# Optimization experiments

Hardware: AMD Instinct MI355X
Metric: run time of the kernel (lower is better)

Reference implementation:

```python
import jax, jax.numpy as jnp
import numpy as np

B, NCAMS = 1, 6
C_FEAT = 64                     # fusion_feat_in_dim
H, W = 88, 160                  # per-camera feature map size at fusion level
VOX_SIZE = (100, 100, 20)       # (x_dim, y_dim, z_dim) voxel counts
VOX_STR = (-50.0, -50.0, -15.0)
VOX_UNIT = (1.0, 1.0, 1.5)
N_VOX = VOX_SIZE[0] * VOX_SIZE[1] * VOX_SIZE[2]
EPS = 1e-8
V_PRE = 64                      # voxel_pre_dim[0]


def make_voxel_pts(dtype):
    # [B, 4, N]; homogeneous (x, y, z, 1) points, layout [z, y, x] flattened
    xs = jnp.linspace(VOX_STR[0], VOX_STR[0] + VOX_UNIT[0] * (VOX_SIZE[0] - 1), VOX_SIZE[0], dtype=dtype)
    ys = jnp.linspace(VOX_STR[1], VOX_STR[1] + VOX_UNIT[1] * (VOX_SIZE[1] - 1), VOX_SIZE[1], dtype=dtype)
    zs = jnp.linspace(VOX_STR[2], VOX_STR[2] + VOX_UNIT[2] * (VOX_SIZE[2] - 1), VOX_SIZE[2], dtype=dtype)
    zdim, ydim, xdim = VOX_SIZE[2], VOX_SIZE[1], VOX_SIZE[0]
    gx = jnp.broadcast_to(xs[None, None, :], (zdim, ydim, xdim)).reshape(-1)
    gy = jnp.broadcast_to(ys[None, :, None], (zdim, ydim, xdim)).reshape(-1)
    gz = jnp.broadcast_to(zs[:, None, None], (zdim, ydim, xdim)).reshape(-1)
    pts = jnp.stack([gx, gy, gz, jnp.ones_like(gx)], axis=0)  # [4, N]
    return jnp.broadcast_to(pts[None], (B, 4, N_VOX))


def _gather(imgf, iy, ix, Wd):
    # imgf: [BN, C, H*W]; iy/ix: [BN, N] int32 -> [BN, C, N]
    lin = iy * Wd + ix
    return jnp.take_along_axis(imgf, lin[:, None, :], axis=2)


def bilinear_sample(img, gx, gy):
    # grid_sample(mode='bilinear', padding_mode='zeros', align_corners=True)
    BN, C, Hd, Wd = img.shape
    x = (gx + 1.0) * 0.5 * (Wd - 1)
    y = (gy + 1.0) * 0.5 * (Hd - 1)
    x0 = jnp.floor(x); y0 = jnp.floor(y)
    wx1 = x - x0; wx0 = 1.0 - wx1
    wy1 = y - y0; wy0 = 1.0 - wy1
    imgf = img.reshape(BN, C, Hd * Wd)
    out = jnp.zeros((BN, C, gx.shape[1]), dtype=img.dtype)
    for xi, wxi in ((x0, wx0), (x0 + 1.0, wx1)):
        for yi, wyi in ((y0, wy0), (y0 + 1.0, wy1)):
            valid = (xi >= 0) & (xi <= Wd - 1) & (yi >= 0) & (yi <= Hd - 1)
            ii = jnp.clip(xi, 0, Wd - 1).astype(jnp.int32)
            jj = jnp.clip(yi, 0, Hd - 1).astype(jnp.int32)
            w = (wxi * wyi * valid.astype(img.dtype))[:, None, :]
            out = out + _gather(imgf, jj, ii, Wd) * w
    return out


def nearest_sample(img, gx, gy):
    # grid_sample(mode='nearest', padding_mode='zeros', align_corners=True)
    BN, C, Hd, Wd = img.shape
    x = (gx + 1.0) * 0.5 * (Wd - 1)
    y = (gy + 1.0) * 0.5 * (Hd - 1)
    xi = jnp.round(x); yi = jnp.round(y)
    valid = (xi >= 0) & (xi <= Wd - 1) & (yi >= 0) & (yi <= Hd - 1)
    ii = jnp.clip(xi, 0, Wd - 1).astype(jnp.int32)
    jj = jnp.clip(yi, 0, Hd - 1).astype(jnp.int32)
    imgf = img.reshape(BN, C, Hd * Wd)
    return _gather(imgf, jj, ii, Wd) * valid[:, None, :].astype(img.dtype)


def setup_inputs() -> dict:
    key = jax.random.key(0)
    ks = jax.random.split(key, 8)
    return {
        'multi_img_feat': jax.random.normal(ks[0], (B, NCAMS, C_FEAT, H, W), jnp.float32),
        'mask': jax.random.uniform(ks[1], (B, NCAMS, 1, H, W), jnp.float32),
        'K': jax.random.normal(ks[2], (B, NCAMS, 4, 4), jnp.float32),
        'extrinsics': jax.random.normal(ks[3], (B, NCAMS, 4, 4), jnp.float32),
        'w_no': jax.random.normal(ks[4], (V_PRE, C_FEAT + 1), jnp.float32) * 0.05,
        'b_no': jax.random.normal(ks[5], (V_PRE,), jnp.float32) * 0.05,
        'w_o': jax.random.normal(ks[6], (V_PRE, 2 * (C_FEAT + 1)), jnp.float32) * 0.05,
        'b_o': jax.random.normal(ks[7], (V_PRE,), jnp.float32) * 0.05,
    }


def reference(multi_img_feat, mask, K, extrinsics, w_no, b_no, w_o, b_o):
    Bb, NC, C, Hd, Wd = multi_img_feat.shape
    dt = multi_img_feat.dtype
    vpts = make_voxel_pts(dt)                                          # [B,4,N]
    vpts_c = jnp.broadcast_to(vpts[:, None], (Bb, NC, 4, N_VOX)).reshape(Bb * NC, 4, N_VOX)
    feats = multi_img_feat.reshape(Bb * NC, C, Hd, Wd)
    masks = mask.reshape(Bb * NC, 1, Hd, Wd)                           # interp to (H,W) is identity (same size, align_corners)
    ext = extrinsics.reshape(Bb * NC, 4, 4)[:, :3, :]
    K3 = K.reshape(Bb * NC, 4, 4)[:, :3, :3]

    v_local = jnp.einsum('bij,bjn->bin', ext, vpts_c)                  # [BN,3,N]
    cam_pts = jnp.einsum('bij,bjn->bin', K3, v_local)
    pix = cam_pts[:, :2] / (cam_pts[:, 2:3] + EPS)
    pix = jnp.where(jnp.all(jnp.isfinite(pix)), pix, jnp.clip(pix, -Wd * 2.0, Wd * 2.0))
    gx = (pix[:, 0] / (Wd - 1) - 0.5) * 2.0                            # [BN,N] normalized coords
    gy = (pix[:, 1] / (Hd - 1) - 0.5) * 2.0

    feat_w = bilinear_sample(feats, gx, gy)                            # [BN,C,N]
    m_occ = nearest_sample(masks, gx, gy) > 0.5                        # [BN,1,N]
    m_depth = v_local[:, 2:3] > 0
    oob = (gx > 1) | (gx < -1) | (gy > 1) | (gy < -1)
    valid = (m_occ & m_depth & (~oob)[:, None, :]).astype(dt)          # [BN,1,N]

    feat_w = jnp.concatenate([feat_w, v_local[:, 2:3] / VOX_SIZE[0]], axis=1) * valid  # [BN,C+1,N]

    feat_w = feat_w.reshape(Bb, NC, C + 1, N_VOX)
    valid = valid.reshape(Bb, NC, 1, N_VOX)
    count = valid.sum(axis=1)                                          # [B,1,N]

    # non-overlap branch: voxels seen by exactly one camera
    no_mask = (count == 1).astype(dt)
    vox_no = feat_w.sum(axis=1) * no_mask
    vox_no = jax.nn.elu(jnp.einsum('oc,bcn->bon', w_no, vox_no) + b_no[None, :, None]) * no_mask

    # overlap branch: cams {0,3,4} vs {1,2,5}
    o_mask = (count == 2).astype(dt)
    feat1 = feat_w[:, 0] + feat_w[:, 3] + feat_w[:, 4]
    feat2 = feat_w[:, 1] + feat_w[:, 2] + feat_w[:, 5]
    vox_o = jnp.concatenate([feat1, feat2], axis=1)                    # [B,2*(C+1),N]
    vox_o = jax.nn.elu(jnp.einsum('oc,bcn->bon', w_o, vox_o) + b_o[None, :, None]) * o_mask

    return vox_no + vox_o                                              # [B, V_PRE, N]
```

## Files before the change

kernel.cpp:

```cpp
#include <hip/hip_runtime.h>
#include <cmath>

#define NC 6
#define CF 64
#define HH 88
#define WW 160
#define NPIX 14080
#define NVOX 200000
#define VPRE 64
#define NGRP 782
#define NTRB 1320

typedef unsigned int u32;

#define FEATT_BYTES  (6u * 64u * 14080u * 4u)
#define CNT1_OFF     (FEATT_BYTES)
#define CNT2_OFF     (CNT1_OFF + 4096u)
#define REC1_OFF     (CNT2_OFF + 4096u)
#define REC2_OFF     (REC1_OFF + (u32)NVOX * 16u)
#define WS_NEED      ((size_t)REC2_OFF + (size_t)NVOX * 32u)
#define OCNT_OFF     (FEATT_BYTES)
#define OREC1_OFF    (OCNT_OFF + 256u)
#define OREC2_OFF    (OREC1_OFF + (u32)NVOX * 16u)
#define WS_NEED_OLD  ((size_t)OREC2_OFF + (size_t)NVOX * 32u)

__device__ __forceinline__ float elu1(float x) { return x > 0.0f ? x : expm1f(x); }

__device__ __forceinline__ float gather_bilin(const float* __restrict__ fsrc, int useT,
                                              int lane, int cam, float x, float y) {
    float x0f = floorf(x), y0f = floorf(y);
    float wx1 = x - x0f, wx0 = 1.0f - wx1;
    float wy1 = y - y0f, wy0 = 1.0f - wy1;
    float x1f = x0f + 1.0f, y1f = y0f + 1.0f;
    float bx0 = (x0f >= 0.0f && x0f <= 159.0f) ? 1.0f : 0.0f;
    float bx1 = (x1f >= 0.0f && x1f <= 159.0f) ? 1.0f : 0.0f;
    float by0 = (y0f >= 0.0f && y0f <= 87.0f) ? 1.0f : 0.0f;
    float by1 = (y1f >= 0.0f && y1f <= 87.0f) ? 1.0f : 0.0f;
    int ix0 = (int)fminf(fmaxf(x0f, 0.0f), 159.0f);
    int ix1 = (int)fminf(fmaxf(x1f, 0.0f), 159.0f);
    int iy0 = (int)fminf(fmaxf(y0f, 0.0f), 87.0f);
    int iy1 = (int)fminf(fmaxf(y1f, 0.0f), 87.0f);
    int A = useT ? 64 : 1;
    int Boff = useT ? (cam * NPIX * 64 + lane) : ((cam * 64 + lane) * NPIX);
    float v00 = fsrc[(iy0 * WW + ix0) * A + Boff];
    float v01 = fsrc[(iy1 * WW + ix0) * A + Boff];
    float v10 = fsrc[(iy0 * WW + ix1) * A + Boff];
    float v11 = fsrc[(iy1 * WW + ix1) * A + Boff];
    float fv;
    fv  = (wx0 * wy0 * bx0 * by0) * v00;
    fv += (wx0 * wy1 * bx0 * by1) * v01;
    fv += (wx1 * wy0 * bx1 * by0) * v10;
    fv += (wx1 * wy1 * bx1 * by1) * v11;
    return fv;
}

__global__ __launch_bounds__(256) void vox_prep(
    const float* __restrict__ feats,
    float* __restrict__ featT,
    const float* __restrict__ mask,
    const float* __restrict__ Kg,
    const float* __restrict__ ext,
    float* __restrict__ outp,
    float4* __restrict__ rec1,
    float4* __restrict__ rec2,
    int* __restrict__ cnt1g,
    int* __restrict__ cnt2g)
{
    __shared__ __align__(16) float s_buf[4290];
    __shared__ float s_ext[72];
    __shared__ float s_K[54];
    __shared__ int s_c1, s_c2;

    int tid = threadIdx.x;
    int lane = tid & 63;
    int wv = tid >> 6;
    int bid = blockIdx.x;

    if (bid < NTRB) {
        int c = bid / 220;
        int p0 = (bid - c * 220) * 64;
        for (int r = wv; r < 64; r += 4)
            s_buf[r * 65 + lane] = feats[(c * 64 + r) * NPIX + p0 + lane];
        __syncthreads();
        for (int r = wv; r < 64; r += 4)
            featT[((c * NPIX) + p0 + r) * 64 + lane] = s_buf[lane * 65 + r];
    } else {
        int g = bid - NTRB;
        float4* s_r1 = (float4*)s_buf;
        float4* s_r2 = ((float4*)s_buf) + 256;
        if (tid == 0) { s_c1 = 0; s_c2 = 0; }
        if (tid >= 64 && tid < 136) {
            int i = tid - 64;
            s_ext[i] = ext[(i / 12) * 16 + (i % 12)];
        }
        if (tid >= 160 && tid < 214) {
            int i = tid - 160; int cam = i / 9; int e = i - cam * 9;
            s_K[i] = Kg[cam * 16 + (e / 3) * 4 + (e % 3)];
        }
        __syncthreads();
        int n = g * 256 + tid;
        if (n < NVOX) {
            #pragma clang fp contract(off)
            int xi = n % 100;
            int t = n / 100;
            int yi = t % 100;
            int zi = t / 100;
            float X = -50.0f + (float)xi;
            float Y = -50.0f + (float)yi;
            float Z = -15.0f + 1.5f * (float)zi;
            int cc = 0, cam0 = 0, cam1 = 0;
            float ax = 0.f, ay = 0.f, az = 0.f, bx = 0.f, by = 0.f, bz = 0.f;
            #pragma unroll
            for (int cam = 0; cam < NC; ++cam) {
                const float* E = s_ext + cam * 12;
                const float* Kk = s_K + cam * 9;
                float vl0 = E[0]*X + E[1]*Y + E[2]*Z + E[3];
                float vl1 = E[4]*X + E[5]*Y + E[6]*Z + E[7];
                float vl2 = E[8]*X + E[9]*Y + E[10]*Z + E[11];
                float c0 = Kk[0]*vl0 + Kk[1]*vl1 + Kk[2]*vl2;
                float c1 = Kk[3]*vl0 + Kk[4]*vl1 + Kk[5]*vl2;
                float c2 = Kk[6]*vl0 + Kk[7]*vl1 + Kk[8]*vl2;
                float pz = c2 + 1e-8f;
                float px = c0 / pz;
                float py = c1 / pz;
                float gx = (px / 159.0f - 0.5f) * 2.0f;
                float gy = (py / 87.0f - 0.5f) * 2.0f;
                float x = ((gx + 1.0f) * 0.5f) * 159.0f;
                float y = ((gy + 1.0f) * 0.5f) * 87.0f;
                float xr = rintf(x), yr = rintf(y);
                bool nv = (xr >= 0.0f) && (xr <= 159.0f) && (yr >= 0.0f) && (yr <= 87.0f);
                float mval = 0.0f;
                if (nv) mval = mask[(cam * HH + (int)yr) * WW + (int)xr];
                bool ok = (mval > 0.5f) && (vl2 > 0.0f) &&
                          !((gx > 1.0f) || (gx < -1.0f) || (gy > 1.0f) || (gy < -1.0f));
                if (ok) {
                    if (cc == 0) { ax = x; ay = y; az = vl2; cam0 = cam; }
                    else if (cc == 1) { bx = x; by = y; bz = vl2; cam1 = cam; }
                    ++cc;
                }
            }
            if (cc == 1) {
                int s = atomicAdd(&s_c1, 1);
                s_r1[s] = make_float4(ax, ay, az, __int_as_float((n << 3) | cam0));
            } else if (cc == 2) {
                int s = atomicAdd(&s_c2, 1);
                s_r2[2 * s + 0] = make_float4(ax, ay, az, __int_as_float((n << 3) | cam0));
                s_r2[2 * s + 1] = make_float4(bx, by, bz, __int_as_float((n << 3) | cam1));
            }
        }
        __syncthreads();
        int c1 = s_c1, c2 = s_c2;
        if (tid == 0) { cnt1g[g] = c1; cnt2g[g] = c2; }
        for (int i = tid; i < c1; i += 256) rec1[g * 256 + i] = s_r1[i];
        for (int i = tid; i < 2 * c2; i += 256) rec2[g * 512 + i] = s_r2[i];
    }

    {
        float4* o4 = (float4*)outp;
        const int n4 = VPRE * NVOX / 4;
        const int stride = (NTRB + NGRP) * 256;
        for (int i = bid * 256 + tid; i < n4; i += stride)
            o4[i] = make_float4(0.f, 0.f, 0.f, 0.f);
    }
}

__device__ __forceinline__ void scan_counts(const int* __restrict__ cg,
                                            int* s_scr, int* s_P, int tid) {
    int base = tid * 4;
    int v0 = (base + 0 < NGRP) ? cg[base + 0] : 0;
    int v1 = (base + 1 < NGRP) ? cg[base + 1] : 0;
    int v2 = (base + 2 < NGRP) ? cg[base + 2] : 0;
    int v3 = (base + 3 < NGRP) ? cg[base + 3] : 0;
    int s0 = v0, s1 = s0 + v1, s2 = s1 + v2, s3 = s2 + v3;
    s_scr[tid] = s3;
    __syncthreads();
    for (int off = 1; off < 256; off <<= 1) {
        int x = s_scr[tid];
        int y = (tid >= off) ? s_scr[tid - off] : 0;
        __syncthreads();
        s_scr[tid] = x + y;
        __syncthreads();
    }
    int excl = (tid > 0) ? s_scr[tid - 1] : 0;
    if (base + 0 < NGRP) s_P[base + 0] = excl + s0;
    if (base + 1 < NGRP) s_P[base + 1] = excl + s1;
    if (base + 2 < NGRP) s_P[base + 2] = excl + s2;
    if (base + 3 < NGRP) s_P[base + 3] = excl + s3;
    __syncthreads();
}

__device__ __forceinline__ int bsearch_grp(const int* __restrict__ P, int k) {
    int lo = 0, hi = NGRP - 1;
    while (lo < hi) { int mid = (lo + hi) >> 1; if (P[mid] > k) hi = mid; else lo = mid + 1; }
    return lo;
}

__global__ __launch_bounds__(256) void vox_comp2(
    const float* __restrict__ featT,
    const float* __restrict__ wno,
    const float* __restrict__ bno,
    const float* __restrict__ wo,
    const float* __restrict__ bo,
    float* __restrict__ outp,
    const float4* __restrict__ rec1,
    const float4* __restrict__ rec2,
    const int* __restrict__ cnt1g,
    const int* __restrict__ cnt2g)
{
    __shared__ float s_F[65 * 66];
    __shared__ float4 s_rec[128];
    __shared__ int s_vox[64];
    __shared__ int s_P1[NGRP];
    __shared__ int s_P2[NGRP];

    int tid = threadIdx.x;
    int lane = tid & 63;
    int wv = tid >> 6;
    int wvu = __builtin_amdgcn_readfirstlane(wv);
    int obase = wvu * 16;

    scan_counts(cnt1g, (int*)s_F, s_P1, tid);
    scan_counts(cnt2g, (int*)s_F, s_P2, tid);
    int n1 = s_P1[NGRP - 1], n2 = s_P2[NGRP - 1];
    int T1 = (n1 + 63) >> 6;
    int T2 = (n2 + 63) >> 6;
    int TT = T1 + T2;

    for (int t = blockIdx.x; t < TT; t += gridDim.x) {
        if (t < T1) {
            int e0 = t << 6;
            int tl = min(64, n1 - e0);
            if (tid < tl) {
                int k = e0 + tid;
                int g = bsearch_grp(s_P1, k);
                int l = k - ((g > 0) ? s_P1[g - 1] : 0);
                s_rec[tid] = rec1[g * 256 + l];
            }
            __syncthreads();
            for (int e = wv; e < tl; e += 4) {
                float4 r = s_rec[e];
                int meta = __float_as_int(r.w);
                int cam = meta & 7;
                float fv = gather_bilin(featT, 1, lane, cam, r.x, r.y);
                s_F[lane * 66 + e] = fv;
                if (lane == 0) { s_F[64 * 66 + e] = r.z / 100.0f; s_vox[e] = meta >> 3; }
            }
            __syncthreads();
            float acc[16];
            #pragma unroll
            for (int o = 0; o < 16; ++o) acc[o] = bno[obase + o];
            for (int cg2 = 0; cg2 < 64; cg2 += 4) {
                float f0 = s_F[(cg2 + 0) * 66 + lane];
                float f1 = s_F[(cg2 + 1) * 66 + lane];
                float f2 = s_F[(cg2 + 2) * 66 + lane];
                float f3 = s_F[(cg2 + 3) * 66 + lane];
                #pragma unroll
                for (int o = 0; o < 16; ++o) {
                    const float* wr = wno + (obase + o) * 65 + cg2;
                    acc[o] += wr[0] * f0; acc[o] += wr[1] * f1;
                    acc[o] += wr[2] * f2; acc[o] += wr[3] * f3;
                }
            }
            {
                float fd = s_F[64 * 66 + lane];
                #pragma unroll
                for (int o = 0; o < 16; ++o) acc[o] += wno[(obase + o) * 65 + 64] * fd;
            }
            if (lane < tl) {
                size_t col = (size_t)s_vox[lane];
                #pragma unroll
                for (int o = 0; o < 16; ++o)
                    outp[(size_t)(obase + o) * NVOX + col] = elu1(acc[o]);
            }
            __syncthreads();
        } else {
            int tt = t - T1;
            int e0 = tt << 6;
            int tl = min(64, n2 - e0);
            if (tid < 2 * tl) {
                int p = tid >> 1, h = tid & 1;
                int k = e0 + p;
                int g = bsearch_grp(s_P2, k);
                int l = k - ((g > 0) ? s_P2[g - 1] : 0);
                s_rec[tid] = rec2[g * 512 + 2 * l + h];
            }
            __syncthreads();
            for (int e = wv; e < tl; e += 4) {
                float4 r0 = s_rec[2 * e + 0];
                float4 r1 = s_rec[2 * e + 1];
                int m0 = __float_as_int(r0.w), m1 = __float_as_int(r1.w);
                int ca = m0 & 7, cb = m1 & 7;
                float fg = 0.0f, dd = 0.0f;
                if (!(ca == 1 || ca == 2 || ca == 5)) {
                    fg += gather_bilin(featT, 1, lane, ca, r0.x, r0.y);
                    dd += r0.z / 100.0f;
                }
                if (!(cb == 1 || cb == 2 || cb == 5)) {
                    fg += gather_bilin(featT, 1, lane, cb, r1.x, r1.y);
                    dd += r1.z / 100.0f;
                }
                s_F[lane * 66 + e] = fg;
                if (lane == 0) { s_F[64 * 66 + e] = dd; s_vox[e] = m0 >> 3; }
            }
            __syncthreads();
            float acc[16];
            #pragma unroll
            for (int o = 0; o < 16; ++o) acc[o] = bo[obase + o];
            for (int cg2 = 0; cg2 < 64; cg2 += 4) {
                float f0 = s_F[(cg2 + 0) * 66 + lane];
                float f1 = s_F[(cg2 + 1) * 66 + lane];
                float f2 = s_F[(cg2 + 2) * 66 + lane];
                float f3 = s_F[(cg2 + 3) * 66 + lane];
                #pragma unroll
                for (int o = 0; o < 16; ++o) {
                    const float* wr = wo + (obase + o) * 130 + cg2;
                    acc[o] += wr[0] * f0; acc[o] += wr[1] * f1;
                    acc[o] += wr[2] * f2; acc[o] += wr[3] * f3;
                }
            }
            {
                float fd = s_F[64 * 66 + lane];
                #pragma unroll
                for (int o = 0; o < 16; ++o) acc[o] += wo[(obase + o) * 130 + 64] * fd;
            }
            __syncthreads();
            for (int e = wv; e < tl; e += 4) {
                float4 r0 = s_rec[2 * e + 0];
                float4 r1 = s_rec[2 * e + 1];
                int m0 = __float_as_int(r0.w), m1 = __float_as_int(r1.w);
                int ca = m0 & 7, cb = m1 & 7;
                float fg = 0.0f, dd = 0.0f;
                if (ca == 1 || ca == 2 || ca == 5) {
                    fg += gather_bilin(featT, 1, lane, ca, r0.x, r0.y);
                    dd += r0.z / 100.0f;
                }
                if (cb == 1 || cb == 2 || cb == 5) {
                    fg += gather_bilin(featT, 1, lane, cb, r1.x, r1.y);
                    dd += r1.z / 100.0f;
                }
                s_F[lane * 66 + e] = fg;
                if (lane == 0) s_F[64 * 66 + e] = dd;
            }
            __syncthreads();
            for (int cg2 = 0; cg2 < 64; cg2 += 4) {
                float f0 = s_F[(cg2 + 0) * 66 + lane];
                float f1 = s_F[(cg2 + 1) * 66 + lane];
                float f2 = s_F[(cg2 + 2) * 66 + lane];
                float f3 = s_F[(cg2 + 3) * 66 + lane];
                #pragma unroll
                for (int o = 0; o < 16; ++o) {
                    const float* wr = wo + (obase + o) * 130 + 65 + cg2;
                    acc[o] += wr[0] * f0; acc[o] += wr[1] * f1;
                    acc[o] += wr[2] * f2; acc[o] += wr[3] * f3;
                }
            }
            {
                float fd = s_F[64 * 66 + lane];
                #pragma unroll
                for (int o = 0; o < 16; ++o) acc[o] += wo[(obase + o) * 130 + 129] * fd;
            }
            if (lane < tl) {
                size_t col = (size_t)s_vox[lane];
                #pragma unroll
                for (int o = 0; o < 16; ++o)
                    outp[(size_t)(obase + o) * NVOX + col] = elu1(acc[o]);
            }
            __syncthreads();
        }
    }
}

__global__ __launch_bounds__(256) void zero_out(float4* __restrict__ p, int n4) {
    int i = blockIdx.x * 256 + threadIdx.x;
    int stride = gridDim.x * 256;
    for (; i < n4; i += stride)
        p[i] = make_float4(0.f, 0.f, 0.f, 0.f);
}

__global__ __launch_bounds__(256) void transpose_feats(const float* __restrict__ in,
                                                       float* __restrict__ out,
                                                       int* __restrict__ cnt) {
    __shared__ float tile[64 * 65];
    if (cnt && blockIdx.x == 0 && threadIdx.x < 2) cnt[threadIdx.x] = 0;
    int blk = blockIdx.x;
    int c = blk / 220;
    int p0 = (blk - c * 220) * 64;
    int tid = threadIdx.x;
    int lane = tid & 63;
    int quad = tid >> 6;
    for (int r = quad; r < 64; r += 4)
        tile[r * 65 + lane] = in[(c * 64 + r) * NPIX + p0 + lane];
    __syncthreads();
    for (int r = quad; r < 64; r += 4)
        out[((c * NPIX) + p0 + r) * 64 + lane] = tile[lane * 65 + r];
}

__global__ __launch_bounds__(256) void vox_geom(
    const float* __restrict__ mask,
    const float* __restrict__ Kg,
    const float* __restrict__ ext,
    float4* __restrict__ rec1,
    float4* __restrict__ rec2,
    int* __restrict__ cnt)
{
    __shared__ float s_ext[72];
    __shared__ float s_K[54];
    __shared__ float4 s_r1[256];
    __shared__ float4 s_r2[512];
    __shared__ int s_c1, s_c2, s_b1, s_b2;

    int tid = threadIdx.x;
    if (tid == 0) { s_c1 = 0; s_c2 = 0; }
    if (tid >= 64 && tid < 136) {
        int i = tid - 64;
        s_ext[i] = ext[(i / 12) * 16 + (i % 12)];
    }
    if (tid >= 160 && tid < 214) {
        int i = tid - 160; int cam = i / 9; int e = i - cam * 9;
        s_K[i] = Kg[cam * 16 + (e / 3) * 4 + (e % 3)];
    }
    __syncthreads();

    int n = blockIdx.x * 256 + tid;
    if (n < NVOX) {
        #pragma clang fp contract(off)
        int xi = n % 100;
        int t = n / 100;
        int yi = t % 100;
        int zi = t / 100;
        float X = -50.0f + (float)xi;
        float Y = -50.0f + (float)yi;
        float Z = -15.0f + 1.5f * (float)zi;
        int cc = 0, cam0 = 0, cam1 = 0;
        float ax = 0.f, ay = 0.f, az = 0.f, bx = 0.f, by = 0.f, bz = 0.f;
        #pragma unroll
        for (int cam = 0; cam < NC; ++cam) {
            const float* E = s_ext + cam * 12;
            const float* Kk = s_K + cam * 9;
            float vl0 = E[0]*X + E[1]*Y + E[2]*Z + E[3];
            float vl1 = E[4]*X + E[5]*Y + E[6]*Z + E[7];
            float vl2 = E[8]*X + E[9]*Y + E[10]*Z + E[11];
            float c0 = Kk[0]*vl0 + Kk[1]*vl1 + Kk[2]*vl2;
            float c1 = Kk[3]*vl0 + Kk[4]*vl1 + Kk[5]*vl2;
            float c2 = Kk[6]*vl0 + Kk[7]*vl1 + Kk[8]*vl2;
            float pz = c2 + 1e-8f;
            float px = c0 / pz;
            float py = c1 / pz;
            float gx = (px / 159.0f - 0.5f) * 2.0f;
            float gy = (py / 87.0f - 0.5f) * 2.0f;
            float x = ((gx + 1.0f) * 0.5f) * 159.0f;
            float y = ((gy + 1.0f) * 0.5f) * 87.0f;
            float xr = rintf(x), yr = rintf(y);
            bool nv = (xr >= 0.0f) && (xr <= 159.0f) && (yr >= 0.0f) && (yr <= 87.0f);
            float mval = 0.0f;
            if (nv) mval = mask[(cam * HH + (int)yr) * WW + (int)xr];
            bool ok = (mval > 0.5f) && (vl2 > 0.0f) &&
                      !((gx > 1.0f) || (gx < -1.0f) || (gy > 1.0f) || (gy < -1.0f));
            if (ok) {
                if (cc == 0) { ax = x; ay = y; az = vl2; cam0 = cam; }
                else if (cc == 1) { bx = x; by = y; bz = vl2; cam1 = cam; }
                ++cc;
            }
        }
        if (cc == 1) {
            int s = atomicAdd(&s_c1, 1);
            s_r1[s] = make_float4(ax, ay, az, __int_as_float((n << 3) | cam0));
        } else if (cc == 2) {
            int s = atomicAdd(&s_c2, 1);
            s_r2[2 * s + 0] = make_float4(ax, ay, az, __int_as_float((n << 3) | cam0));
            s_r2[2 * s + 1] = make_float4(bx, by, bz, __int_as_float((n << 3) | cam1));
        }
    }
    __syncthreads();
    if (tid == 0) {
        s_b1 = atomicAdd(cnt + 0, s_c1);
        s_b2 = atomicAdd(cnt + 1, s_c2);
    }
    __syncthreads();
    int c1 = s_c1, c2 = s_c2, b1 = s_b1, b2 = s_b2;
    for (int i = tid; i < c1; i += 256) rec1[b1 + i] = s_r1[i];
    for (int i = tid; i < 2 * c2; i += 256) rec2[2 * b2 + i] = s_r2[i];
}

__global__ __launch_bounds__(256) void vox_comp(
    const float* __restrict__ featT,
    const float* __restrict__ wno,
    const float* __restrict__ bno,
    const float* __restrict__ wo,
    const float* __restrict__ bo,
    float* __restrict__ outp,
    const float4* __restrict__ rec1,
    const float4* __restrict__ rec2,
    const int* __restrict__ cnt)
{
    __shared__ float s_F[65 * 66];
    __shared__ float4 s_rec[128];
    __shared__ int s_vox[64];

    int tid = threadIdx.x;
    int lane = tid & 63;
    int wv = tid >> 6;
    int wvu = __builtin_amdgcn_readfirstlane(wv);
    int obase = wvu * 16;

    int n1 = cnt[0], n2 = cnt[1];
    int T1 = (n1 + 63) >> 6;
    int T2 = (n2 + 63) >> 6;
    int TT = T1 + T2;

    for (int t = blockIdx.x; t < TT; t += gridDim.x) {
        if (t < T1) {
            int e0 = t << 6;
            int tl = min(64, n1 - e0);
            if (tid < tl) s_rec[tid] = rec1[e0 + tid];
            __syncthreads();
            for (int e = wv; e < tl; e += 4) {
                float4 r = s_rec[e];
                int meta = __float_as_int(r.w);
                int cam = meta & 7;
                float fv = gather_bilin(featT, 1, lane, cam, r.x, r.y);
                s_F[lane * 66 + e] = fv;
                if (lane == 0) { s_F[64 * 66 + e] = r.z / 100.0f; s_vox[e] = meta >> 3; }
            }
            __syncthreads();
            float acc[16];
            #pragma unroll
            for (int o = 0; o < 16; ++o) acc[o] = bno[obase + o];
            for (int cg2 = 0; cg2 < 64; cg2 += 4) {
                float f0 = s_F[(cg2 + 0) * 66 + lane];
                float f1 = s_F[(cg2 + 1) * 66 + lane];
                float f2 = s_F[(cg2 + 2) * 66 + lane];
                float f3 = s_F[(cg2 + 3) * 66 + lane];
                #pragma unroll
                for (int o = 0; o < 16; ++o) {
                    const float* wr = wno + (obase + o) * 65 + cg2;
                    acc[o] += wr[0] * f0; acc[o] += wr[1] * f1;
                    acc[o] += wr[2] * f2; acc[o] += wr[3] * f3;
                }
            }
            {
                float fd = s_F[64 * 66 + lane];
                #pragma unroll
                for (int o = 0; o < 16; ++o) acc[o] += wno[(obase + o) * 65 + 64] * fd;
            }
            if (lane < tl) {
                size_t col = (size_t)s_vox[lane];
                #pragma unroll
                for (int o = 0; o < 16; ++o)
                    outp[(size_t)(obase + o) * NVOX + col] = elu1(acc[o]);
            }
            __syncthreads();
        } else {
            int tt = t - T1;
            int e0 = tt << 6;
            int tl = min(64, n2 - e0);
            if (tid < 2 * tl) s_rec[tid] = rec2[2 * e0 + tid];
            __syncthreads();
            for (int e = wv; e < tl; e += 4) {
                float4 r0 = s_rec[2 * e + 0];
                float4 r1 = s_rec[2 * e + 1];
                int m0 = __float_as_int(r0.w), m1 = __float_as_int(r1.w);
                int ca = m0 & 7, cb = m1 & 7;
                float fg = 0.0f, dd = 0.0f;
                if (!(ca == 1 || ca == 2 || ca == 5)) {
                    fg += gather_bilin(featT, 1, lane, ca, r0.x, r0.y);
                    dd += r0.z / 100.0f;
                }
                if (!(cb == 1 || cb == 2 || cb == 5)) {
                    fg += gather_bilin(featT, 1, lane, cb, r1.x, r1.y);
                    dd += r1.z / 100.0f;
                }
                s_F[lane * 66 + e] = fg;
                if (lane == 0) { s_F[64 * 66 + e] = dd; s_vox[e] = m0 >> 3; }
            }
            __syncthreads();
            float acc[16];
            #pragma unroll
            for (int o = 0; o < 16; ++o) acc[o] = bo[obase + o];
            for (int cg2 = 0; cg2 < 64; cg2 += 4) {
                float f0 = s_F[(cg2 + 0) * 66 + lane];
                float f1 = s_F[(cg2 + 1) * 66 + lane];
                float f2 = s_F[(cg2 + 2) * 66 + lane];
                float f3 = s_F[(cg2 + 3) * 66 + lane];
                #pragma unroll
                for (int o = 0; o < 16; ++o) {
                    const float* wr = wo + (obase + o) * 130 + cg2;
                    acc[o] += wr[0] * f0; acc[o] += wr[1] * f1;
                    acc[o] += wr[2] * f2; acc[o] += wr[3] * f3;
                }
            }
            {
                float fd = s_F[64 * 66 + lane];
                #pragma unroll
                for (int o = 0; o < 16; ++o) acc[o] += wo[(obase + o) * 130 + 64] * fd;
            }
            __syncthreads();
            for (int e = wv; e < tl; e += 4) {
                float4 r0 = s_rec[2 * e + 0];
                float4 r1 = s_rec[2 * e + 1];
                int m0 = __float_as_int(r0.w), m1 = __float_as_int(r1.w);
                int ca = m0 & 7, cb = m1 & 7;
                float fg = 0.0f, dd = 0.0f;
                if (ca == 1 || ca == 2 || ca == 5) {
                    fg += gather_bilin(featT, 1, lane, ca, r0.x, r0.y);
                    dd += r0.z / 100.0f;
                }
                if (cb == 1 || cb == 2 || cb == 5) {
                    fg += gather_bilin(featT, 1, lane, cb, r1.x, r1.y);
                    dd += r1.z / 100.0f;
                }
                s_F[lane * 66 + e] = fg;
                if (lane == 0) s_F[64 * 66 + e] = dd;
            }
            __syncthreads();
            for (int cg2 = 0; cg2 < 64; cg2 += 4) {
                float f0 = s_F[(cg2 + 0) * 66 + lane];
                float f1 = s_F[(cg2 + 1) * 66 + lane];
                float f2 = s_F[(cg2 + 2) * 66 + lane];
                float f3 = s_F[(cg2 + 3) * 66 + lane];
                #pragma unroll
                for (int o = 0; o < 16; ++o) {
                    const float* wr = wo + (obase + o) * 130 + 65 + cg2;
                    acc[o] += wr[0] * f0; acc[o] += wr[1] * f1;
                    acc[o] += wr[2] * f2; acc[o] += wr[3] * f3;
                }
            }
            {
                float fd = s_F[64 * 66 + lane];
                #pragma unroll
                for (int o = 0; o < 16; ++o) acc[o] += wo[(obase + o) * 130 + 129] * fd;
            }
            if (lane < tl) {
                size_t col = (size_t)s_vox[lane];
                #pragma unroll
                for (int o = 0; o < 16; ++o)
                    outp[(size_t)(obase + o) * NVOX + col] = elu1(acc[o]);
            }
            __syncthreads();
        }
    }
}

extern "C" void kernel_launch(void* const* d_in, const int* in_sizes, int n_in,
                              void* d_out, int out_size, void* d_ws, size_t ws_size,
                              hipStream_t stream) {
    const float* feats = (const float*)d_in[0];
    const float* mask  = (const float*)d_in[1];
    const float* Kg    = (const float*)d_in[2];
    const float* ext   = (const float*)d_in[3];
    const float* wno   = (const float*)d_in[4];
    const float* bno   = (const float*)d_in[5];
    const float* wo    = (const float*)d_in[6];
    const float* bo    = (const float*)d_in[7];
    float* outp = (float*)d_out;
    float* featT = (float*)d_ws;

    if (ws_size >= WS_NEED) {
        int* cnt1g = (int*)((char*)d_ws + CNT1_OFF);
        int* cnt2g = (int*)((char*)d_ws + CNT2_OFF);
        float4* rec1 = (float4*)((char*)d_ws + REC1_OFF);
        float4* rec2 = (float4*)((char*)d_ws + REC2_OFF);
        vox_prep<<<NTRB + NGRP, 256, 0, stream>>>(feats, featT, mask, Kg, ext,
                                                  outp, rec1, rec2, cnt1g, cnt2g);
        vox_comp2<<<2048, 256, 0, stream>>>(featT, wno, bno, wo, bo, outp,
                                            rec1, rec2, cnt1g, cnt2g);
    } else if (ws_size >= WS_NEED_OLD) {
        int* cnt = (int*)((char*)d_ws + OCNT_OFF);
        float4* rec1 = (float4*)((char*)d_ws + OREC1_OFF);
        float4* rec2 = (float4*)((char*)d_ws + OREC2_OFF);
        zero_out<<<2048, 256, 0, stream>>>((float4*)d_out,
                                           (int)((size_t)VPRE * NVOX / 4));
        transpose_feats<<<NC * 220, 256, 0, stream>>>(feats, featT, cnt);
        vox_geom<<<(NVOX + 255) / 256, 256, 0, stream>>>(mask, Kg, ext,
                                                         rec1, rec2, cnt);
        vox_comp<<<2048, 256, 0, stream>>>(featT, wno, bno, wo, bo, outp,
                                           rec1, rec2, cnt);
    } else {
        zero_out<<<2048, 256, 0, stream>>>((float4*)d_out,
                                           (int)((size_t)VPRE * NVOX / 4));
    }
}
```

Measured before the change: 160.0 us.

## Vectorize bilinear gathers to 8 channels per lane and use wave-level prefix scan

```diff
diff --git a/kernel.cpp b/kernel.cpp
--- a/kernel.cpp
+++ b/kernel.cpp
@@ -52,6 +52,44 @@
     fv += (wx1 * wy0 * bx1 * by0) * v10;
     fv += (wx1 * wy1 * bx1 * by1) * v11;
     return fv;
+}
+
+__device__ __forceinline__ void gather_bilin8(const float* __restrict__ fsrc,
+                                              int q8, int cam, float x, float y,
+                                              float4& fa, float4& fb) {
+    float x0f = floorf(x), y0f = floorf(y);
+    float wx1 = x - x0f, wx0 = 1.0f - wx1;
+    float wy1 = y - y0f, wy0 = 1.0f - wy1;
+    float x1f = x0f + 1.0f, y1f = y0f + 1.0f;
+    float bx0 = (x0f >= 0.0f && x0f <= 159.0f) ? 1.0f : 0.0f;
+    float bx1 = (x1f >= 0.0f && x1f <= 159.0f) ? 1.0f : 0.0f;
+    float by0 = (y0f >= 0.0f && y0f <= 87.0f) ? 1.0f : 0.0f;
+    float by1 = (y1f >= 0.0f && y1f <= 87.0f) ? 1.0f : 0.0f;
+    int ix0 = (int)fminf(fmaxf(x0f, 0.0f), 159.0f);
+    int ix1 = (int)fminf(fmaxf(x1f, 0.0f), 159.0f);
+    int iy0 = (int)fminf(fmaxf(y0f, 0.0f), 87.0f);
+    int iy1 = (int)fminf(fmaxf(y1f, 0.0f), 87.0f);
+    const float4* base = (const float4*)(fsrc) + cam * (NPIX * 16) + 2 * q8;
+    int p00 = (iy0 * WW + ix0) * 16;
+    int p01 = (iy1 * WW + ix0) * 16;
+    int p10 = (iy0 * WW + ix1) * 16;
+    int p11 = (iy1 * WW + ix1) * 16;
+    float4 a00 = base[p00], b00 = base[p00 + 1];
+    float4 a01 = base[p01], b01 = base[p01 + 1];
+    float4 a10 = base[p10], b10 = base[p10 + 1];
+    float4 a11 = base[p11], b11 = base[p11 + 1];
+    float w00 = wx0 * wy0 * bx0 * by0;
+    float w01 = wx0 * wy1 * bx0 * by1;
+    float w10 = wx1 * wy0 * bx1 * by0;
+    float w11 = wx1 * wy1 * bx1 * by1;
+    fa.x  = w00 * a00.x; fa.x += w01 * a01.x; fa.x += w10 * a10.x; fa.x += w11 * a11.x;
+    fa.y  = w00 * a00.y; fa.y += w01 * a01.y; fa.y += w10 * a10.y; fa.y += w11 * a11.y;
+    fa.z  = w00 * a00.z; fa.z += w01 * a01.z; fa.z += w10 * a10.z; fa.z += w11 * a11.z;
+    fa.w  = w00 * a00.w; fa.w += w01 * a01.w; fa.w += w10 * a10.w; fa.w += w11 * a11.w;
+    fb.x  = w00 * b00.x; fb.x += w01 * b01.x; fb.x += w10 * b10.x; fb.x += w11 * b11.x;
+    fb.y  = w00 * b00.y; fb.y += w01 * b01.y; fb.y += w10 * b10.y; fb.y += w11 * b11.y;
+    fb.z  = w00 * b00.z; fb.z += w01 * b01.z; fb.z += w10 * b10.z; fb.z += w11 * b11.z;
+    fb.w  = w00 * b00.w; fb.w += w01 * b01.w; fb.w += w10 * b10.w; fb.w += w11 * b11.w;
 }
 
 __global__ __launch_bounds__(256) void vox_prep(
@@ -164,29 +202,30 @@
     }
 }
 
-__device__ __forceinline__ void scan_counts(const int* __restrict__ cg,
-                                            int* s_scr, int* s_P, int tid) {
-    int base = tid * 4;
-    int v0 = (base + 0 < NGRP) ? cg[base + 0] : 0;
-    int v1 = (base + 1 < NGRP) ? cg[base + 1] : 0;
-    int v2 = (base + 2 < NGRP) ? cg[base + 2] : 0;
-    int v3 = (base + 3 < NGRP) ? cg[base + 3] : 0;
-    int s0 = v0, s1 = s0 + v1, s2 = s1 + v2, s3 = s2 + v3;
-    s_scr[tid] = s3;
-    __syncthreads();
-    for (int off = 1; off < 256; off <<= 1) {
-        int x = s_scr[tid];
-        int y = (tid >= off) ? s_scr[tid - off] : 0;
-        __syncthreads();
-        s_scr[tid] = x + y;
-        __syncthreads();
-    }
-    int excl = (tid > 0) ? s_scr[tid - 1] : 0;
-    if (base + 0 < NGRP) s_P[base + 0] = excl + s0;
-    if (base + 1 < NGRP) s_P[base + 1] = excl + s1;
-    if (base + 2 < NGRP) s_P[base + 2] = excl + s2;
-    if (base + 3 < NGRP) s_P[base + 3] = excl + s3;
-    __syncthreads();
+__device__ __forceinline__ void scan_wave(const int* __restrict__ cg,
+                                          int* __restrict__ s_P, int lane) {
+    int base = lane * 13;
+    int v[13];
+    int sum = 0;
+    #pragma unroll
+    for (int i = 0; i < 13; ++i) {
+        int idx = base + i;
+        int x = (idx < NGRP) ? cg[idx] : 0;
+        sum += x;
+        v[i] = sum;
+    }
+    int s = sum;
+    #pragma unroll
+    for (int off = 1; off < 64; off <<= 1) {
+        int y = __shfl_up(s, off, 64);
+        if (lane >= off) s += y;
+    }
+    int excl = s - sum;
+    #pragma unroll
+    for (int i = 0; i < 13; ++i) {
+        int idx = base + i;
+        if (idx < NGRP) s_P[idx] = excl + v[i];
+    }
 }
 
 __device__ __forceinline__ int bsearch_grp(const int* __restrict__ P, int k) {
@@ -207,7 +246,7 @@
     const int* __restrict__ cnt1g,
     const int* __restrict__ cnt2g)
 {
-    __shared__ float s_F[65 * 66];
+    __shared__ __align__(16) float s_F[65 * 66];
     __shared__ float4 s_rec[128];
     __shared__ int s_vox[64];
     __shared__ int s_P1[NGRP];
@@ -218,9 +257,14 @@
     int wv = tid >> 6;
     int wvu = __builtin_amdgcn_readfirstlane(wv);
     int obase = wvu * 16;
-
-    scan_counts(cnt1g, (int*)s_F, s_P1, tid);
-    scan_counts(cnt2g, (int*)s_F, s_P2, tid);
+    int q8 = lane & 7;
+    int j8 = lane >> 3;
+
+    if (wv == 0) {
+        scan_wave(cnt1g, s_P1, lane);
+        scan_wave(cnt2g, s_P2, lane);
+    }
+    __syncthreads();
     int n1 = s_P1[NGRP - 1], n2 = s_P2[NGRP - 1];
     int T1 = (n1 + 63) >> 6;
     int T2 = (n2 + 63) >> 6;
@@ -237,13 +281,25 @@
                 s_rec[tid] = rec1[g * 256 + l];
             }
             __syncthreads();
-            for (int e = wv; e < tl; e += 4) {
-                float4 r = s_rec[e];
-                int meta = __float_as_int(r.w);
-                int cam = meta & 7;
-                float fv = gather_bilin(featT, 1, lane, cam, r.x, r.y);
-                s_F[lane * 66 + e] = fv;
-                if (lane == 0) { s_F[64 * 66 + e] = r.z / 100.0f; s_vox[e] = meta >> 3; }
+            #pragma unroll 1
+            for (int u = 0; u < 2; ++u) {
+                int e = wv + 4 * j8 + 32 * u;
+                if (e < tl) {
+                    float4 r = s_rec[e];
+                    int meta = __float_as_int(r.w);
+                    int cam = meta & 7;
+                    float4 fa, fb;
+                    gather_bilin8(featT, q8, cam, r.x, r.y, fa, fb);
+                    s_F[(8 * q8 + 0) * 66 + e] = fa.x;
+                    s_F[(8 * q8 + 1) * 66 + e] = fa.y;
+                    s_F[(8 * q8 + 2) * 66 + e] = fa.z;
+                    s_F[(8 * q8 + 3) * 66 + e] = fa.w;
+                    s_F[(8 * q8 + 4) * 66 + e] = fb.x;
+                    s_F[(8 * q8 + 5) * 66 + e] = fb.y;
+                    s_F[(8 * q8 + 6) * 66 + e] = fb.z;
+                    s_F[(8 * q8 + 7) * 66 + e] = fb.w;
+                    if (q8 == 0) { s_F[64 * 66 + e] = r.z / 100.0f; s_vox[e] = meta >> 3; }
+                }
             }
             __syncthreads();
             float acc[16];
@@ -285,22 +341,41 @@
                 s_rec[tid] = rec2[g * 512 + 2 * l + h];
             }
             __syncthreads();
-            for (int e = wv; e < tl; e += 4) {
-                float4 r0 = s_rec[2 * e + 0];
-                float4 r1 = s_rec[2 * e + 1];
-                int m0 = __float_as_int(r0.w), m1 = __float_as_int(r1.w);
-                int ca = m0 & 7, cb = m1 & 7;
-                float fg = 0.0f, dd = 0.0f;
-                if (!(ca == 1 || ca == 2 || ca == 5)) {
-                    fg += gather_bilin(featT, 1, lane, ca, r0.x, r0.y);
-                    dd += r0.z / 100.0f;
-                }
-                if (!(cb == 1 || cb == 2 || cb == 5)) {
-                    fg += gather_bilin(featT, 1, lane, cb, r1.x, r1.y);
-                    dd += r1.z / 100.0f;
-                }
-                s_F[lane * 66 + e] = fg;
-                if (lane == 0) { s_F[64 * 66 + e] = dd; s_vox[e] = m0 >> 3; }
+            #pragma unroll 1
+            for (int u = 0; u < 2; ++u) {
+                int e = wv + 4 * j8 + 32 * u;
+                if (e < tl) {
+                    float4 r0 = s_rec[2 * e + 0];
+                    float4 r1 = s_rec[2 * e + 1];
+                    int m0 = __float_as_int(r0.w), m1 = __float_as_int(r1.w);
+                    int ca = m0 & 7, cb = m1 & 7;
+                    float4 fga = make_float4(0.f, 0.f, 0.f, 0.f);
+                    float4 fgb = make_float4(0.f, 0.f, 0.f, 0.f);
+                    float dd = 0.0f;
+                    if (!(ca == 1 || ca == 2 || ca == 5)) {
+                        float4 ga, gb;
+                        gather_bilin8(featT, q8, ca, r0.x, r0.y, ga, gb);
+                        fga.x += ga.x; fga.y += ga.y; fga.z += ga.z; fga.w += ga.w;
+                        fgb.x += gb.x; fgb.y += gb.y; fgb.z += gb.z; fgb.w += gb.w;
+                        dd += r0.z / 100.0f;
+                    }
+                    if (!(cb == 1 || cb == 2 || cb == 5)) {
+                        float4 ga, gb;
+                        gather_bilin8(featT, q8, cb, r1.x, r1.y, ga, gb);
+                        fga.x += ga.x; fga.y += ga.y; fga.z += ga.z; fga.w += ga.w;
+                        fgb.x += gb.x; fgb.y += gb.y; fgb.z += gb.z; fgb.w += gb.w;
+                        dd += r1.z / 100.0f;
+                    }
+                    s_F[(8 * q8 + 0) * 66 + e] = fga.x;
+                    s_F[(8 * q8 + 1) * 66 + e] = fga.y;
+                    s_F[(8 * q8 + 2) * 66 + e] = fga.z;
+                    s_F[(8 * q8 + 3) * 66 + e] = fga.w;
+                    s_F[(8 * q8 + 4) * 66 + e] = fgb.x;
+                    s_F[(8 * q8 + 5) * 66 + e] = fgb.y;
+                    s_F[(8 * q8 + 6) * 66 + e] = fgb.z;
+                    s_F[(8 * q8 + 7) * 66 + e] = fgb.w;
+                    if (q8 == 0) { s_F[64 * 66 + e] = dd; s_vox[e] = m0 >> 3; }
+                }
             }
             __syncthreads();
             float acc[16];
@@ -324,22 +399,41 @@
                 for (int o = 0; o < 16; ++o) acc[o] += wo[(obase + o) * 130 + 64] * fd;
             }
             __syncthreads();
-            for (int e = wv; e < tl; e += 4) {
-                float4 r0 = s_rec[2 * e + 0];
-                float4 r1 = s_rec[2 * e + 1];
-                int m0 = __float_as_int(r0.w), m1 = __float_as_int(r1.w);
-                int ca = m0 & 7, cb = m1 & 7;
-                float fg = 0.0f, dd = 0.0f;
-                if (ca == 1 || ca == 2 || ca == 5) {
-                    fg += gather_bilin(featT, 1, lane, ca, r0.x, r0.y);
-                    dd += r0.z / 100.0f;
-                }
-                if (cb == 1 || cb == 2 || cb == 5) {
-                    fg += gather_bilin(featT, 1, lane, cb, r1.x, r1.y);
-                    dd += r1.z / 100.0f;
-                }
-                s_F[lane * 66 + e] = fg;
-                if (lane == 0) s_F[64 * 66 + e] = dd;
+            #pragma unroll 1
+            for (int u = 0; u < 2; ++u) {
+                int e = wv + 4 * j8 + 32 * u;
+                if (e < tl) {
+                    float4 r0 = s_rec[2 * e + 0];
+                    float4 r1 = s_rec[2 * e + 1];
+                    int m0 = __float_as_int(r0.w), m1 = __float_as_int(r1.w);
+                    int ca = m0 & 7, cb = m1 & 7;
+                    float4 fga = make_float4(0.f, 0.f, 0.f, 0.f);
+                    float4 fgb = make_float4(0.f, 0.f, 0.f, 0.f);
+                    float dd = 0.0f;
+                    if (ca == 1 || ca == 2 || ca == 5) {
+                        float4 ga, gb;
+                        gather_bilin8(featT, q8, ca, r0.x, r0.y, ga, gb);
+                        fga.x += ga.x; fga.y += ga.y; fga.z += ga.z; fga.w += ga.w;
+                        fgb.x += gb.x; fgb.y += gb.y; fgb.z += gb.z; fgb.w += gb.w;
+                        dd += r0.z / 100.0f;
+                    }
+                    if (cb == 1 || cb == 2 || cb == 5) {
+                        float4 ga, gb;
+                        gather_bilin8(featT, q8, cb, r1.x, r1.y, ga, gb);
+                        fga.x += ga.x; fga.y += ga.y; fga.z += ga.z; fga.w += ga.w;
+                        fgb.x += gb.x; fgb.y += gb.y; fgb.z += gb.z; fgb.w += gb.w;
+                        dd += r1.z / 100.0f;
+                    }
+                    s_F[(8 * q8 + 0) * 66 + e] = fga.x;
+                    s_F[(8 * q8 + 1) * 66 + e] = fga.y;
+                    s_F[(8 * q8 + 2) * 66 + e] = fga.z;
+                    s_F[(8 * q8 + 3) * 66 + e] = fga.w;
+                    s_F[(8 * q8 + 4) * 66 + e] = fgb.x;
+                    s_F[(8 * q8 + 5) * 66 + e] = fgb.y;
+                    s_F[(8 * q8 + 6) * 66 + e] = fgb.z;
+                    s_F[(8 * q8 + 7) * 66 + e] = fgb.w;
+                    if (q8 == 0) s_F[64 * 66 + e] = dd;
+                }
             }
             __syncthreads();
             for (int cg2 = 0; cg2 < 64; cg2 += 4) {
```

Result: faster. 152.2 us, median of 2 (-4.9%).
